# Optimization experiments

Measured on AMD Instinct MI355X. Metric: run time of the kernel, lower is better.

Reference implementation:

```python
import jax, jax.numpy as jnp
import numpy as np

INPUT_SIZE, HIDDEN_SIZE, MEMORY_SIZE, SEQ_LEN, THETA = 512, 1024, 256, 4096, 4096.0
BATCH = 8


def _expm(M):
    # scaling-and-squaring Taylor expm (float64), replaces scipy cont2discrete's expm
    nrm = np.linalg.norm(M, 1)
    s = max(0, int(np.ceil(np.log2(max(nrm, 1.0)))) + 4)
    A = M / (2.0 ** s)
    E = np.eye(M.shape[0])
    T = np.eye(M.shape[0])
    for k in range(1, 24):
        T = T @ A / k
        E = E + T
    for _ in range(s):
        E = E @ E
    return E


def _lmu_H():
    # continuous-time Legendre state-space matrices
    Q = np.arange(MEMORY_SIZE, dtype=np.float64).reshape(-1, 1)
    R = (2.0 * Q + 1.0) / THETA
    i, j = np.meshgrid(Q.ravel(), Q.ravel(), indexing="ij")
    A = R * np.where(i < j, -1.0, (-1.0) ** (i - j + 1))
    B = R * (-1.0) ** Q
    # zero-order-hold discretization with dt=1: expm([[A,B],[0,0]])
    aug = np.zeros((MEMORY_SIZE + 1, MEMORY_SIZE + 1))
    aug[:MEMORY_SIZE, :MEMORY_SIZE] = A
    aug[:MEMORY_SIZE, MEMORY_SIZE:] = B
    Md = _expm(aug)
    Ad = Md[:MEMORY_SIZE, :MEMORY_SIZE].astype(np.float32)
    Bd = Md[:MEMORY_SIZE, MEMORY_SIZE:].astype(np.float32)
    # impulse response: H[:, t] = Ad^t @ Bd  (matches torch impulse() in float32)
    H = np.empty((MEMORY_SIZE, SEQ_LEN), dtype=np.float32)
    h = Bd[:, 0]
    for t in range(SEQ_LEN):
        H[:, t] = h
        h = Ad @ h
    return H


def setup_inputs():
    key = jax.random.key(0)
    k1, k2, k3, k4, k5 = jax.random.split(key, 5)
    x = jax.random.normal(k1, (BATCH, SEQ_LEN, INPUT_SIZE), jnp.float32)
    W_u_w = jax.random.normal(k2, (1, INPUT_SIZE), jnp.float32) / np.float32(np.sqrt(INPUT_SIZE))
    W_u_b = jax.random.normal(k3, (1,), jnp.float32) * 0.01
    W_h_w = jax.random.normal(k4, (HIDDEN_SIZE, MEMORY_SIZE + INPUT_SIZE), jnp.float32) / np.float32(np.sqrt(MEMORY_SIZE + INPUT_SIZE))
    W_h_b = jax.random.normal(k5, (HIDDEN_SIZE,), jnp.float32) * 0.01
    H = jnp.asarray(_lmu_H())
    return {"x": x, "W_u_w": W_u_w, "W_u_b": W_u_b, "W_h_w": W_h_w, "W_h_b": W_h_b, "H": H}


def reference(x, W_u_w, W_u_b, W_h_w, W_h_b, H):
    B, S, D = x.shape
    # u_t = relu(W_u x_t)  -> [B, S, 1]
    u = jax.nn.relu(jnp.einsum("bsd,od->bso", x, W_u_w) + W_u_b)
    # FFT long convolution of u with impulse response H (linear conv via 2S padding)
    fft_u = jnp.fft.rfft(u.transpose(0, 2, 1), n=2 * S, axis=-1)  # [B, 1, S+1]
    fft_H = jnp.fft.rfft(H, n=2 * S, axis=-1)                     # [M, S+1]
    m = jnp.fft.irfft(fft_u * fft_H[None], n=2 * S, axis=-1)[:, :, :S]  # [B, M, S]
    m = m.transpose(0, 2, 1)                                      # [B, S, M]
    # h_t = relu(W_h [m_t; x_t])
    h = jax.nn.relu(jnp.einsum("bsk,hk->bsh", jnp.concatenate([m, x], axis=-1), W_h_w) + W_h_b)
    return h, h[:, -1, :]
```

## Files before the change

kernel.cpp:

```cpp
#include <hip/hip_runtime.h>

typedef _Float16 half8 __attribute__((ext_vector_type(8)));
typedef float f32x4 __attribute__((ext_vector_type(4)));

#define SEQ   4096
#define DIN   512
#define HID   1024
#define KMEM  256
#define NB    8
#define KC    768
#define VP    4352
#define OUT_H_ELEMS 33554432ull

__device__ __forceinline__ void load_lds16(const void* g, void* l) {
  __builtin_amdgcn_global_load_lds(
      (const __attribute__((address_space(1))) unsigned int*)g,
      (__attribute__((address_space(3))) unsigned int*)l, 16, 0, 0);
}

__global__ __launch_bounds__(256) void u_kernel(
    const float* __restrict__ x, const float* __restrict__ Wu,
    const float* __restrict__ Wub,
    const float* __restrict__ Hf, const float* __restrict__ Wf,
    _Float16* __restrict__ xh, _Float16* __restrict__ v2,
    _Float16* __restrict__ Hh, _Float16* __restrict__ Wh)
{
  int tid_g = blockIdx.x * 256 + threadIdx.x;
  if (tid_g < KMEM * SEQ) Hh[tid_g] = (_Float16)Hf[tid_g];
  if (tid_g < HID * KC)   Wh[tid_g] = (_Float16)Wf[tid_g];
  if (tid_g < NB * 8 * 256) {
    int b2 = tid_g >> 11, rem = tid_g & 2047, p = rem >> 8, z = rem & 255;
    int t = (z < p) ? z : 4096 + z;
    v2[((size_t)b2 * 8 + p) * VP + t] = (_Float16)0.f;
  }

  int w = threadIdx.x >> 6, lane = threadIdx.x & 63;
  int row = blockIdx.x * 4 + w;
  const float4* xr = (const float4*)(x + (size_t)row * DIN);
  const float4* wr = (const float4*)Wu;
  float4 a0 = xr[lane * 2], a1 = xr[lane * 2 + 1];
  float4 w0 = wr[lane * 2], w1 = wr[lane * 2 + 1];
  float dot = a0.x * w0.x + a0.y * w0.y + a0.z * w0.z + a0.w * w0.w
            + a1.x * w1.x + a1.y * w1.y + a1.z * w1.z + a1.w * w1.w;
  half8 hv;
  hv[0] = (_Float16)a0.x; hv[1] = (_Float16)a0.y;
  hv[2] = (_Float16)a0.z; hv[3] = (_Float16)a0.w;
  hv[4] = (_Float16)a1.x; hv[5] = (_Float16)a1.y;
  hv[6] = (_Float16)a1.z; hv[7] = (_Float16)a1.w;
  *((half8*)(xh + (size_t)row * DIN + lane * 8)) = hv;
  #pragma unroll
  for (int off = 32; off > 0; off >>= 1) dot += __shfl_xor(dot, off);
  float u = dot + Wub[0];
  u = u > 0.f ? u : 0.f;
  if (lane < 8) {
    int s = row & (SEQ - 1), b = row >> 12;
    v2[(size_t)b * 8 * VP + (size_t)lane * VP + (4095 - s + lane)] = (_Float16)u;
  }
}

__global__ __launch_bounds__(256) void conv_kernel(
    const _Float16* __restrict__ Hh, const _Float16* __restrict__ v2,
    _Float16* __restrict__ mh)
{
  __shared__ _Float16 Bs[2][128 * 32];
  __shared__ _Float16 Aw[2][8 * 104];
  int cb = blockIdx.x;
  int b = cb >> 1, kt = cb & 1;
  int by = blockIdx.y;
  int its = (by & 1) ? (63 - (by >> 1)) : (by >> 1);
  int s0 = its * 64, k0 = kt * 128;
  int tid = threadIdx.x;
  int w = tid >> 6, lane = tid & 63;
  int wr = w >> 1, wc = w & 1;
  int lm = lane & 15, q = lane >> 4;
  const _Float16* v2b = v2 + (size_t)b * 8 * VP;
  int gbase0 = 4032 - s0;

  int aoffs[2];
  #pragma unroll
  for (int mi = 0; mi < 2; mi++) {
    int X = wr * 32 + mi * 16 + lm;
    int p = (X + 1) & 7;
    aoffs[mi] = p * 104 + (63 - X + p) + q * 8;
  }
  int boffs[4];
  #pragma unroll
  for (int ni = 0; ni < 4; ni++)
    boffs[ni] = (wc * 64 + ni * 16 + lm) * 32 + q * 8;

  int ap = tid / 13, aidx = tid - ap * 13;

  f32x4 acc[2][4] = {};
  int iters = 2 * (its + 1);

  {
    if (tid < 104)
      load_lds16(v2b + (size_t)ap * VP + gbase0 + aidx * 8, Aw[0] + tid * 8);
    #pragma unroll
    for (int p2 = 0; p2 < 2; p2++) {
      int c = p2 * 256 + tid;
      int col = c >> 2, ch = c & 3;
      load_lds16(Hh + (size_t)(k0 + col) * SEQ + ch * 8, Bs[0] + (size_t)c * 8);
    }
  }

  for (int it = 0; it < iters; ++it) {
    int buf = it & 1;
    __syncthreads();
    if (it + 1 < iters) {
      int r0 = (it + 1) * 32;
      if (tid < 104)
        load_lds16(v2b + (size_t)ap * VP + gbase0 + r0 + aidx * 8, Aw[buf ^ 1] + tid * 8);
      #pragma unroll
      for (int p2 = 0; p2 < 2; p2++) {
        int c = p2 * 256 + tid;
        int col = c >> 2, ch = c & 3;
        load_lds16(Hh + (size_t)(k0 + col) * SEQ + r0 + ch * 8, Bs[buf ^ 1] + (size_t)c * 8);
      }
    }
    half8 af[2], bf[4];
    #pragma unroll
    for (int mi = 0; mi < 2; mi++) af[mi] = *((const half8*)(Aw[buf] + aoffs[mi]));
    #pragma unroll
    for (int ni = 0; ni < 4; ni++) bf[ni] = *((const half8*)(Bs[buf] + boffs[ni]));
    #pragma unroll
    for (int mi = 0; mi < 2; mi++)
      #pragma unroll
      for (int ni = 0; ni < 4; ni++)
        acc[mi][ni] = __builtin_amdgcn_mfma_f32_16x16x32_f16(af[mi], bf[ni], acc[mi][ni], 0, 0, 0);
  }
  size_t rowbase = (size_t)b * SEQ;
  #pragma unroll
  for (int mi = 0; mi < 2; mi++) {
    #pragma unroll
    for (int ni = 0; ni < 4; ni++) {
      int kout = k0 + wc * 64 + ni * 16 + lm;
      #pragma unroll
      for (int r = 0; r < 4; r++) {
        int sout = s0 + wr * 32 + mi * 16 + q * 4 + r;
        mh[(rowbase + sout) * KMEM + kout] = (_Float16)acc[mi][ni][r];
      }
    }
  }
}

__global__ __launch_bounds__(256) void h_kernel(
    const _Float16* __restrict__ mh, const _Float16* __restrict__ xh,
    const _Float16* __restrict__ Wh, const float* __restrict__ Whb,
    float* __restrict__ out)
{
  __shared__ _Float16 As[2][128 * 32];
  __shared__ _Float16 Bs[2][128 * 32];
  int id = blockIdx.y * 8 + blockIdx.x;
  int xcd = id & 7;
  int j = id >> 3;
  int mt = (j >> 3) * 8 + xcd;
  int nt = j & 7;
  int tid = threadIdx.x, w = tid >> 6, lane = tid & 63;
  int wr = w >> 1, wc = w & 1, lm = lane & 15, q = lane >> 4;

  f32x4 acc[4][4] = {};
  {
    #pragma unroll
    for (int p2 = 0; p2 < 2; p2++) {
      int c = p2 * 256 + tid;
      int row = c >> 2, ch = c & 3;
      size_t rg = (size_t)mt * 128 + row;
      load_lds16(mh + rg * KMEM + ch * 8, As[0] + (size_t)c * 8);
      load_lds16(Wh + (size_t)(nt * 128 + row) * KC + ch * 8, Bs[0] + (size_t)c * 8);
    }
  }
  for (int it = 0; it < 24; ++it) {
    int buf = it & 1;
    __syncthreads();
    if (it + 1 < 24) {
      int kk = (it + 1) * 32;
      #pragma unroll
      for (int p2 = 0; p2 < 2; p2++) {
        int c = p2 * 256 + tid;
        int row = c >> 2, ch = c & 3;
        size_t rg = (size_t)mt * 128 + row;
        const _Float16* srcA = (kk < KMEM)
            ? (mh + rg * KMEM + kk + ch * 8)
            : (xh + rg * DIN + (kk - KMEM) + ch * 8);
        load_lds16(srcA, As[buf ^ 1] + (size_t)c * 8);
        load_lds16(Wh + (size_t)(nt * 128 + row) * KC + kk + ch * 8,
                   Bs[buf ^ 1] + (size_t)c * 8);
      }
    }
    half8 af[4], bf[4];
    #pragma unroll
    for (int mi = 0; mi < 4; mi++)
      af[mi] = *((const half8*)(As[buf] + (wr * 64 + mi * 16 + lm) * 32 + q * 8));
    #pragma unroll
    for (int ni = 0; ni < 4; ni++)
      bf[ni] = *((const half8*)(Bs[buf] + (wc * 64 + ni * 16 + lm) * 32 + q * 8));
    #pragma unroll
    for (int mi = 0; mi < 4; mi++)
      #pragma unroll
      for (int ni = 0; ni < 4; ni++)
        acc[mi][ni] = __builtin_amdgcn_mfma_f32_16x16x32_f16(af[mi], bf[ni], acc[mi][ni], 0, 0, 0);
  }
  #pragma unroll
  for (int ni = 0; ni < 4; ni++) {
    int colg = nt * 128 + wc * 64 + ni * 16 + lm;
    float bias = Whb[colg];
    #pragma unroll
    for (int mi = 0; mi < 4; mi++) {
      #pragma unroll
      for (int r = 0; r < 4; r++) {
        int rowg = mt * 128 + wr * 64 + mi * 16 + q * 4 + r;
        float v = acc[mi][ni][r] + bias;
        v = v > 0.f ? v : 0.f;
        out[(size_t)rowg * HID + colg] = v;
        if ((rowg & (SEQ - 1)) == SEQ - 1)
          out[OUT_H_ELEMS + (size_t)(rowg >> 12) * HID + colg] = v;
      }
    }
  }
}

extern "C" void kernel_launch(void* const* d_in, const int* in_sizes, int n_in,
                              void* d_out, int out_size, void* d_ws, size_t ws_size,
                              hipStream_t stream) {
  const float* x   = (const float*)d_in[0];
  const float* Wu  = (const float*)d_in[1];
  const float* Wub = (const float*)d_in[2];
  const float* Whw = (const float*)d_in[3];
  const float* Whb = (const float*)d_in[4];
  const float* Hf  = (const float*)d_in[5];
  float* out = (float*)d_out;

  char* ws = (char*)d_ws;
  _Float16* Hh = (_Float16*)(ws);
  _Float16* Wh = (_Float16*)(ws + 2097152);
  _Float16* v2 = (_Float16*)(ws + 3670016);
  _Float16* xh = (_Float16*)(ws + 4227072);
  _Float16* mh = (_Float16*)(ws + 37781504);

  u_kernel<<<dim3(8192), dim3(256), 0, stream>>>(x, Wu, Wub, Hf, Whw, xh, v2, Hh, Wh);
  conv_kernel<<<dim3(16, 64), dim3(256), 0, stream>>>(Hh, v2, mh);
  h_kernel<<<dim3(8, 256), dim3(256), 0, stream>>>(mh, xh, Wh, Whb, out);
}
```

Before: 334.3 us.

## Restructure h_kernel to 256x256 tiles with 4-stage LDS pipeline

The output GEMM kernel now uses 512-thread blocks computing 256x256 tiles instead of 128x128 tiles. It stages three K-slices ahead in a 4-deep LDS ring buffer, with explicit vmcnt waits and split barriers. MFMA sections are wrapped in s_setprio to raise priority, and the block-to-XCD mapping is remapped. The aim is better operand reuse and more overlap of global loads with MFMA. The cost is higher register and LDS use (64KB A+B per block), which limits occupancy and makes the hand-managed synchronisation more fragile.

```diff
diff --git a/kernel.cpp b/kernel.cpp
--- a/kernel.cpp
+++ b/kernel.cpp
@@ -144,72 +144,101 @@
   }
 }
 
-__global__ __launch_bounds__(256) void h_kernel(
+__global__ __launch_bounds__(512, 2) void h_kernel(
     const _Float16* __restrict__ mh, const _Float16* __restrict__ xh,
     const _Float16* __restrict__ Wh, const float* __restrict__ Whb,
     float* __restrict__ out)
 {
-  __shared__ _Float16 As[2][128 * 32];
-  __shared__ _Float16 Bs[2][128 * 32];
-  int id = blockIdx.y * 8 + blockIdx.x;
-  int xcd = id & 7;
-  int j = id >> 3;
-  int mt = (j >> 3) * 8 + xcd;
-  int nt = j & 7;
-  int tid = threadIdx.x, w = tid >> 6, lane = tid & 63;
-  int wr = w >> 1, wc = w & 1, lm = lane & 15, q = lane >> 4;
-
-  f32x4 acc[4][4] = {};
-  {
-    #pragma unroll
-    for (int p2 = 0; p2 < 2; p2++) {
-      int c = p2 * 256 + tid;
-      int row = c >> 2, ch = c & 3;
-      size_t rg = (size_t)mt * 128 + row;
-      load_lds16(mh + rg * KMEM + ch * 8, As[0] + (size_t)c * 8);
-      load_lds16(Wh + (size_t)(nt * 128 + row) * KC + ch * 8, Bs[0] + (size_t)c * 8);
-    }
-  }
-  for (int it = 0; it < 24; ++it) {
-    int buf = it & 1;
-    __syncthreads();
-    if (it + 1 < 24) {
-      int kk = (it + 1) * 32;
-      #pragma unroll
-      for (int p2 = 0; p2 < 2; p2++) {
-        int c = p2 * 256 + tid;
-        int row = c >> 2, ch = c & 3;
-        size_t rg = (size_t)mt * 128 + row;
-        const _Float16* srcA = (kk < KMEM)
-            ? (mh + rg * KMEM + kk + ch * 8)
-            : (xh + rg * DIN + (kk - KMEM) + ch * 8);
-        load_lds16(srcA, As[buf ^ 1] + (size_t)c * 8);
-        load_lds16(Wh + (size_t)(nt * 128 + row) * KC + kk + ch * 8,
-                   Bs[buf ^ 1] + (size_t)c * 8);
-      }
-    }
-    half8 af[4], bf[4];
-    #pragma unroll
-    for (int mi = 0; mi < 4; mi++)
-      af[mi] = *((const half8*)(As[buf] + (wr * 64 + mi * 16 + lm) * 32 + q * 8));
-    #pragma unroll
-    for (int ni = 0; ni < 4; ni++)
-      bf[ni] = *((const half8*)(Bs[buf] + (wc * 64 + ni * 16 + lm) * 32 + q * 8));
-    #pragma unroll
-    for (int mi = 0; mi < 4; mi++)
-      #pragma unroll
-      for (int ni = 0; ni < 4; ni++)
-        acc[mi][ni] = __builtin_amdgcn_mfma_f32_16x16x32_f16(af[mi], bf[ni], acc[mi][ni], 0, 0, 0);
-  }
-  #pragma unroll
-  for (int ni = 0; ni < 4; ni++) {
-    int colg = nt * 128 + wc * 64 + ni * 16 + lm;
+  __shared__ _Float16 ldsA[4][8192];
+  __shared__ _Float16 ldsB[4][8192];
+
+  int id = blockIdx.x;
+  int wgid = (id & 7) * 64 + (id >> 3);
+  int mt = wgid >> 2, nt = wgid & 3;
+
+  int tid = threadIdx.x;
+  int w = tid >> 6, lane = tid & 63;
+  int wr = w >> 2, wc = w & 3;
+  int lm = lane & 15, q = lane >> 4;
+
+  size_t offAm[2], offAx[2], offB[2];
+  #pragma unroll
+  for (int r = 0; r < 2; ++r) {
+    int c = r * 512 + tid;
+    int row = c >> 2, j = c & 3;
+    offAm[r] = ((size_t)mt * 256 + row) * KMEM + j * 8;
+    offAx[r] = ((size_t)mt * 256 + row) * DIN  + j * 8;
+    offB[r]  = ((size_t)nt * 256 + row) * KC   + j * 8;
+  }
+
+#define STAGE_ROUND(kk, rr) do {                                              \
+    int kb_ = (kk) * 32;                                                      \
+    int c_ = (rr) * 512 + tid;                                                \
+    const _Float16* sa_ = (kb_ < KMEM) ? (mh + offAm[rr] + kb_)               \
+                                       : (xh + offAx[rr] + (kb_ - KMEM));     \
+    load_lds16(sa_, &ldsA[(kk) & 3][c_ * 8]);                                 \
+    load_lds16(Wh + offB[rr] + kb_, &ldsB[(kk) & 3][c_ * 8]);                 \
+  } while (0)
+
+  f32x4 acc[8][4] = {};
+
+  #pragma unroll
+  for (int kk = 0; kk < 3; ++kk) { STAGE_ROUND(kk, 0); STAGE_ROUND(kk, 1); }
+  asm volatile("s_waitcnt vmcnt(8)" ::: "memory");
+  __builtin_amdgcn_s_barrier();
+  asm volatile("" ::: "memory");
+
+  for (int k = 0; k < 24; ++k) {
+    const _Float16* la = ldsA[k & 3];
+    const _Float16* lb = ldsB[k & 3];
+    half8 bf[4];
+    #pragma unroll
+    for (int qd = 0; qd < 2; ++qd) {
+      half8 af[4];
+      #pragma unroll
+      for (int m2 = 0; m2 < 4; ++m2)
+        af[m2] = *((const half8*)(la + (wr * 128 + (qd * 4 + m2) * 16 + lm) * 32 + q * 8));
+      if (qd == 0) {
+        #pragma unroll
+        for (int ni = 0; ni < 4; ++ni)
+          bf[ni] = *((const half8*)(lb + (wc * 64 + ni * 16 + lm) * 32 + q * 8));
+      }
+      if (k < 21) STAGE_ROUND(k + 3, qd);
+
+      asm volatile("" ::: "memory");
+      __builtin_amdgcn_s_barrier();
+      asm volatile("" ::: "memory");
+
+      __builtin_amdgcn_s_setprio(1);
+      #pragma unroll
+      for (int m2 = 0; m2 < 4; ++m2)
+        #pragma unroll
+        for (int ni = 0; ni < 4; ++ni)
+          acc[qd * 4 + m2][ni] = __builtin_amdgcn_mfma_f32_16x16x32_f16(
+              af[m2], bf[ni], acc[qd * 4 + m2][ni], 0, 0, 0);
+      __builtin_amdgcn_s_setprio(0);
+
+      if (qd == 1) {
+        if (k < 21)      asm volatile("s_waitcnt vmcnt(8)" ::: "memory");
+        else if (k == 21) asm volatile("s_waitcnt vmcnt(4)" ::: "memory");
+        else              asm volatile("s_waitcnt vmcnt(0)" ::: "memory");
+      }
+      asm volatile("" ::: "memory");
+      __builtin_amdgcn_s_barrier();
+      asm volatile("" ::: "memory");
+    }
+  }
+#undef STAGE_ROUND
+
+  #pragma unroll
+  for (int ni = 0; ni < 4; ++ni) {
+    int colg = nt * 256 + wc * 64 + ni * 16 + lm;
     float bias = Whb[colg];
     #pragma unroll
-    for (int mi = 0; mi < 4; mi++) {
-      #pragma unroll
-      for (int r = 0; r < 4; r++) {
-        int rowg = mt * 128 + wr * 64 + mi * 16 + q * 4 + r;
+    for (int mi = 0; mi < 8; ++mi) {
+      #pragma unroll
+      for (int r = 0; r < 4; ++r) {
+        int rowg = mt * 256 + wr * 128 + mi * 16 + q * 4 + r;
         float v = acc[mi][ni][r] + bias;
         v = v > 0.f ? v : 0.f;
         out[(size_t)rowg * HID + colg] = v;
@@ -240,5 +269,5 @@
 
   u_kernel<<<dim3(8192), dim3(256), 0, stream>>>(x, Wu, Wub, Hf, Whw, xh, v2, Hh, Wh);
   conv_kernel<<<dim3(16, 64), dim3(256), 0, stream>>>(Hh, v2, mh);
-  h_kernel<<<dim3(8, 256), dim3(256), 0, stream>>>(mh, xh, Wh, Whb, out);
-}
+  h_kernel<<<dim3(512), dim3(512), 0, stream>>>(mh, xh, Wh, Whb, out);
+}
```

After: 342.8 us. 2.5% more time.

## Enlarge conv kernel tiles to 128x128 with 64-deep K and swizzled LDS

Applied to the files above, without the earlier changes.

The Toeplitz-style convolution GEMM moves from 64-row by 32-deep tiles to 128-row by 64-deep tiles, so each warp holds a 4x4 MFMA accumulator block. Each loaded H and u-window element is reused for more MFMAs, and there are fewer barriers per unit of work. The B tile in LDS gets an XOR swizzle to avoid bank conflicts. The grid becomes a 1-D launch of 512 blocks that pairs short and long triangular tiles, with a launch-bounds occupancy hint. The cost is fewer blocks to spread over the CUs, a coarser triangular load imbalance, and higher register pressure.

```diff
diff --git a/kernel.cpp b/kernel.cpp
--- a/kernel.cpp
+++ b/kernel.cpp
@@ -58,49 +58,53 @@
   }
 }
 
-__global__ __launch_bounds__(256) void conv_kernel(
+__global__ __launch_bounds__(256, 3) void conv_kernel(
     const _Float16* __restrict__ Hh, const _Float16* __restrict__ v2,
     _Float16* __restrict__ mh)
 {
-  __shared__ _Float16 Bs[2][128 * 32];
-  __shared__ _Float16 Aw[2][8 * 104];
-  int cb = blockIdx.x;
+  __shared__ _Float16 Bs[2][128 * 64];
+  __shared__ _Float16 Aw[2][8 * 208];
+  int g = blockIdx.x;
+  int cb = g & 15;
   int b = cb >> 1, kt = cb & 1;
-  int by = blockIdx.y;
-  int its = (by & 1) ? (63 - (by >> 1)) : (by >> 1);
-  int s0 = its * 64, k0 = kt * 128;
+  int jj = g >> 4;
+  int its = (jj < 16) ? jj : (47 - jj);
+  int s0 = its * 128, k0 = kt * 128;
   int tid = threadIdx.x;
   int w = tid >> 6, lane = tid & 63;
   int wr = w >> 1, wc = w & 1;
   int lm = lane & 15, q = lane >> 4;
   const _Float16* v2b = v2 + (size_t)b * 8 * VP;
-  int gbase0 = 4032 - s0;
-
-  int aoffs[2];
-  #pragma unroll
-  for (int mi = 0; mi < 2; mi++) {
-    int X = wr * 32 + mi * 16 + lm;
+  int gb = 3968 - s0;
+
+  int aoffs[4];
+  #pragma unroll
+  for (int mi = 0; mi < 4; mi++) {
+    int X = wr * 64 + mi * 16 + lm;
     int p = (X + 1) & 7;
-    aoffs[mi] = p * 104 + (63 - X + p) + q * 8;
+    aoffs[mi] = p * 208 + (127 - X + p) + q * 8;
   }
   int boffs[4];
   #pragma unroll
-  for (int ni = 0; ni < 4; ni++)
-    boffs[ni] = (wc * 64 + ni * 16 + lm) * 32 + q * 8;
-
-  int ap = tid / 13, aidx = tid - ap * 13;
-
-  f32x4 acc[2][4] = {};
+  for (int ni = 0; ni < 4; ni++) {
+    int col = wc * 64 + ni * 16 + lm;
+    boffs[ni] = col * 64 + ((q ^ (lm & 7)) << 3);
+  }
+
+  int ap = tid / 26, aidx = tid - ap * 26;
+
+  f32x4 acc[4][4] = {};
   int iters = 2 * (its + 1);
 
   {
-    if (tid < 104)
-      load_lds16(v2b + (size_t)ap * VP + gbase0 + aidx * 8, Aw[0] + tid * 8);
-    #pragma unroll
-    for (int p2 = 0; p2 < 2; p2++) {
+    if (tid < 208)
+      load_lds16(v2b + (size_t)ap * VP + gb + aidx * 8, Aw[0] + tid * 8);
+    #pragma unroll
+    for (int p2 = 0; p2 < 4; p2++) {
       int c = p2 * 256 + tid;
-      int col = c >> 2, ch = c & 3;
-      load_lds16(Hh + (size_t)(k0 + col) * SEQ + ch * 8, Bs[0] + (size_t)c * 8);
+      int col = c >> 3, sl = c & 7;
+      load_lds16(Hh + (size_t)(k0 + col) * SEQ + ((sl ^ (col & 7)) << 3),
+                 Bs[0] + (size_t)c * 8);
     }
   }
 
@@ -108,36 +112,42 @@
     int buf = it & 1;
     __syncthreads();
     if (it + 1 < iters) {
-      int r0 = (it + 1) * 32;
-      if (tid < 104)
-        load_lds16(v2b + (size_t)ap * VP + gbase0 + r0 + aidx * 8, Aw[buf ^ 1] + tid * 8);
-      #pragma unroll
-      for (int p2 = 0; p2 < 2; p2++) {
+      int r0 = (it + 1) * 64;
+      if (tid < 208)
+        load_lds16(v2b + (size_t)ap * VP + gb + r0 + aidx * 8, Aw[buf ^ 1] + tid * 8);
+      #pragma unroll
+      for (int p2 = 0; p2 < 4; p2++) {
         int c = p2 * 256 + tid;
-        int col = c >> 2, ch = c & 3;
-        load_lds16(Hh + (size_t)(k0 + col) * SEQ + r0 + ch * 8, Bs[buf ^ 1] + (size_t)c * 8);
-      }
-    }
-    half8 af[2], bf[4];
-    #pragma unroll
-    for (int mi = 0; mi < 2; mi++) af[mi] = *((const half8*)(Aw[buf] + aoffs[mi]));
-    #pragma unroll
-    for (int ni = 0; ni < 4; ni++) bf[ni] = *((const half8*)(Bs[buf] + boffs[ni]));
-    #pragma unroll
-    for (int mi = 0; mi < 2; mi++)
+        int col = c >> 3, sl = c & 7;
+        load_lds16(Hh + (size_t)(k0 + col) * SEQ + r0 + ((sl ^ (col & 7)) << 3),
+                   Bs[buf ^ 1] + (size_t)c * 8);
+      }
+    }
+    #pragma unroll
+    for (int kq = 0; kq < 2; kq++) {
+      half8 af[4], bf[4];
+      #pragma unroll
+      for (int mi = 0; mi < 4; mi++)
+        af[mi] = *((const half8*)(Aw[buf] + aoffs[mi] + kq * 32));
       #pragma unroll
       for (int ni = 0; ni < 4; ni++)
-        acc[mi][ni] = __builtin_amdgcn_mfma_f32_16x16x32_f16(af[mi], bf[ni], acc[mi][ni], 0, 0, 0);
+        bf[ni] = *((const half8*)(Bs[buf] + (boffs[ni] ^ (kq << 5))));
+      #pragma unroll
+      for (int mi = 0; mi < 4; mi++)
+        #pragma unroll
+        for (int ni = 0; ni < 4; ni++)
+          acc[mi][ni] = __builtin_amdgcn_mfma_f32_16x16x32_f16(af[mi], bf[ni], acc[mi][ni], 0, 0, 0);
+    }
   }
   size_t rowbase = (size_t)b * SEQ;
   #pragma unroll
-  for (int mi = 0; mi < 2; mi++) {
+  for (int mi = 0; mi < 4; mi++) {
     #pragma unroll
     for (int ni = 0; ni < 4; ni++) {
       int kout = k0 + wc * 64 + ni * 16 + lm;
       #pragma unroll
       for (int r = 0; r < 4; r++) {
-        int sout = s0 + wr * 32 + mi * 16 + q * 4 + r;
+        int sout = s0 + wr * 64 + mi * 16 + q * 4 + r;
         mh[(rowbase + sout) * KMEM + kout] = (_Float16)acc[mi][ni][r];
       }
     }
@@ -239,6 +249,6 @@
   _Float16* mh = (_Float16*)(ws + 37781504);
 
   u_kernel<<<dim3(8192), dim3(256), 0, stream>>>(x, Wu, Wub, Hf, Whw, xh, v2, Hh, Wh);
-  conv_kernel<<<dim3(16, 64), dim3(256), 0, stream>>>(Hh, v2, mh);
+  conv_kernel<<<dim3(512), dim3(256), 0, stream>>>(Hh, v2, mh);
   h_kernel<<<dim3(8, 256), dim3(256), 0, stream>>>(mh, xh, Wh, Whb, out);
 }
```

After: 327.2 us. -2.1%, faster.
